# Kernel optimization log

Measured on AMD Instinct MI355X. Metric: run time of the kernel, lower is better.

Reference implementation:

```python
import jax, jax.numpy as jnp
import numpy as np

D_MODEL = 1024
NUM_HEADS = 16
D_K = D_MODEL // NUM_HEADS
B, L = 2, 2048
NEG = -1e9


def setup_inputs() -> dict:
    key = jax.random.key(0)
    ks = jax.random.split(key, 11)
    s = 1.0 / np.sqrt(D_MODEL)
    inp = {
        "Q": jax.random.normal(ks[0], (B, L, D_MODEL), jnp.float32),
        "K": jax.random.normal(ks[1], (B, L, D_MODEL), jnp.float32),
        "V": jax.random.normal(ks[2], (B, L, D_MODEL), jnp.float32),
        # causal mask: True = valid (attend), False = masked
        "mask": jnp.tril(jnp.ones((L, L), bool))[None, None],
        # torch nn.Linear weights stored [out, in]
        "Wq": jax.random.normal(ks[3], (D_MODEL, D_MODEL), jnp.float32) * s,
        "bq": jnp.zeros((D_MODEL,), jnp.float32),
        "Wk": jax.random.normal(ks[4], (D_MODEL, D_MODEL), jnp.float32) * s,
        "bk": jnp.zeros((D_MODEL,), jnp.float32),
        "Wv": jax.random.normal(ks[5], (D_MODEL, D_MODEL), jnp.float32) * s,
        "bv": jnp.zeros((D_MODEL,), jnp.float32),
        "Wo": jax.random.normal(ks[6], (D_MODEL, D_MODEL), jnp.float32) * s,
        "bo": jnp.zeros((D_MODEL,), jnp.float32),
    }
    return inp


def _split_heads(x):  # [B,L,D] -> [B,H,L,d_k]
    b, l, _ = x.shape
    return x.reshape(b, l, NUM_HEADS, D_K).transpose(0, 2, 1, 3)


def reference(Q, K, V, mask, Wq, bq, Wk, bk, Wv, bv, Wo, bo):
    # linear projections (torch Linear: x @ W.T + b)
    q = _split_heads(Q @ Wq.T + bq)
    k = _split_heads(K @ Wk.T + bk)
    v = _split_heads(V @ Wv.T + bv)
    scores = jnp.einsum("bhqd,bhkd->bhqk", q, k) / jnp.sqrt(jnp.float32(D_K))
    scores = jnp.where(mask, scores, NEG)
    probs = jax.nn.softmax(scores, axis=-1)  # dropout inactive at inference
    attn = jnp.einsum("bhqk,bhkd->bhqd", probs, v)
    b, h, l, dk = attn.shape
    o_in = attn.transpose(0, 2, 1, 3).reshape(b, l, D_MODEL)
    return o_in @ Wo.T + bo
```

## Files before the change

kernel.cpp:

```cpp
#include <hip/hip_runtime.h>
#include <stdint.h>

#define D_MODEL 1024
#define NH 16
#define DK 64
#define BBATCH 2
#define LL 2048
#define SCALE_LOG2E 0.1803368801111244f

typedef unsigned short bfu;
typedef __attribute__((ext_vector_type(8))) short bf16x8;
typedef __attribute__((ext_vector_type(4))) float f32x4;

union BF8 { uint32_t w[4]; bf16x8 v; };

__device__ __forceinline__ bfu f2bf(float f) {
    union { float f; uint32_t u; } a; a.f = f;
    uint32_t r = a.u + 0x7FFF + ((a.u >> 16) & 1);
    return (bfu)(r >> 16);
}
__device__ __forceinline__ uint32_t pktrunc(float hi, float lo) {
    return __builtin_amdgcn_perm(__float_as_uint(hi), __float_as_uint(lo), 0x07060302);
}

__device__ __forceinline__ void gload_lds16(const void* g, void* l) {
    __builtin_amdgcn_global_load_lds(
        (const __attribute__((address_space(1))) void*)g,
        (__attribute__((address_space(3))) void*)l, 16, 0, 0);
}

__device__ __forceinline__ int swz(int R, int G) {
    return R * 64 + (((G ^ (R & 7))) << 3);
}

__global__ __launch_bounds__(256) void cvt_all(
    const float4* __restrict__ s0, const float4* __restrict__ s1, const float4* __restrict__ s2,
    const float4* __restrict__ s3, const float4* __restrict__ s4, const float4* __restrict__ s5,
    const float4* __restrict__ s6, ushort4* __restrict__ dst)
{
    int i = blockIdx.x * 256 + threadIdx.x;
    const float4* s; int off;
    float sc = 1.0f;
    if (i < (3 << 20)) {
        int t = i >> 20; s = (t == 0) ? s0 : ((t == 1) ? s1 : s2);
        off = i & ((1 << 20) - 1);
    } else {
        int j = i - (3 << 20);
        int t = j >> 18; s = (t == 0) ? s3 : ((t == 1) ? s4 : ((t == 2) ? s5 : s6));
        if (t == 0) sc = SCALE_LOG2E;
        off = j & ((1 << 18) - 1);
    }
    float4 v = s[off];
    ushort4 o;
    o.x = f2bf(v.x * sc); o.y = f2bf(v.y * sc); o.z = f2bf(v.z * sc); o.w = f2bf(v.w * sc);
    dst[i] = o;
}

#define BM 128
#define BN 128
#define BKK 64

__device__ __forceinline__ int kperm(int k) {
    return (((k >> 4) & 1) << 5) | (((k >> 2) & 3) << 3) | (((k >> 5) & 1) << 2) | (k & 3);
}

__global__ __launch_bounds__(256, 2) void gemm_proj(
    const bfu* __restrict__ Qb, const bfu* __restrict__ Kb, const bfu* __restrict__ Vb,
    const bfu* __restrict__ Wq, const bfu* __restrict__ Wk, const bfu* __restrict__ Wv,
    const float* __restrict__ bq, const float* __restrict__ bk, const float* __restrict__ bv,
    bfu* __restrict__ qp, bfu* __restrict__ kp, bfu* __restrict__ vt)
{
    const int z = blockIdx.z;
    const bfu* A = (z == 0) ? Qb : ((z == 1) ? Kb : Vb);
    const bfu* B = (z == 0) ? Wq : ((z == 1) ? Wk : Wv);
    const float* bias = (z == 0) ? bq : ((z == 1) ? bk : bv);
    const float bsc = (z == 0) ? SCALE_LOG2E : 1.0f;
    bfu* out = (z == 0) ? qp : ((z == 1) ? kp : vt);

    __shared__ __align__(16) bfu As[BM * BKK];
    __shared__ __align__(16) bfu Bs[BN * BKK];

    const int t = threadIdx.x;
    const int lane = t & 63;
    const int wave = t >> 6;
    const int wm = wave & 1, wn = wave >> 1;
    const int tm = blockIdx.y * BM, tn = blockIdx.x * BN;
    const int lr = lane & 15, quad = lane >> 4;

    f32x4 acc[4][4];
    for (int i = 0; i < 4; i++) for (int j = 0; j < 4; j++) acc[i][j] = (f32x4){0.f, 0.f, 0.f, 0.f};

    for (int kt = 0; kt < 1024; kt += BKK) {
        for (int it = 0; it < 4; ++it) {
            int c = t + it * 256;
            int row = c >> 3, gx = (c & 7) ^ (row & 7);
            gload_lds16(&A[(size_t)(tm + row) * 1024 + kt + gx * 8], &As[(size_t)c * 8]);
        }
        for (int it = 0; it < 4; ++it) {
            int c = t + it * 256;
            int row = c >> 3, gx = (c & 7) ^ (row & 7);
            gload_lds16(&B[(size_t)(tn + row) * 1024 + kt + gx * 8], &Bs[(size_t)c * 8]);
        }
        __syncthreads();
        for (int kx = 0; kx < 2; kx++) {
            bf16x8 a[4], b[4];
            for (int i = 0; i < 4; i++)
                a[i] = *(const bf16x8*)&As[swz(wm * 64 + i * 16 + lr, kx * 4 + quad)];
            for (int i = 0; i < 4; i++)
                b[i] = *(const bf16x8*)&Bs[swz(wn * 64 + i * 16 + lr, kx * 4 + quad)];
            for (int mt = 0; mt < 4; mt++)
                for (int nt = 0; nt < 4; nt++)
                    acc[mt][nt] = __builtin_amdgcn_mfma_f32_16x16x32_bf16(a[mt], b[nt], acc[mt][nt], 0, 0, 0);
        }
        __syncthreads();
    }

    for (int mt = 0; mt < 4; mt++)
        for (int nt = 0; nt < 4; nt++)
            for (int r = 0; r < 4; r++) {
                int m = tm + wm * 64 + mt * 16 + quad * 4 + r;
                int n = tn + wn * 64 + nt * 16 + lr;
                float v = acc[mt][nt][r] + bias[n] * bsc;
                int b_ = m >> 11, l = m & 2047;
                int h = n >> 6, d = n & 63;
                if (z < 2)
                    out[((size_t)((b_ * NH + h) * LL + l)) * DK + d] = f2bf(v);
                else {
                    int lp = (l & ~63) | kperm(l & 63);
                    out[((size_t)((b_ * NH + h) * DK + d)) * LL + lp] = f2bf(v);
                }
            }
}

__global__ __launch_bounds__(256, 2) void attn_kernel(
    const bfu* __restrict__ qp, const bfu* __restrict__ kp, const bfu* __restrict__ vtp,
    bfu* __restrict__ attn)
{
    const int id = blockIdx.x;
    const int bh = (id & 7) | (((id >> 3) & 3) << 3);
    const int band = 31 - (id >> 5);
    const int b_ = bh >> 4, h = bh & 15;
    const int t = threadIdx.x;
    const int lane = t & 63, w = t >> 6;
    const int hw = w & 1;
    const int jh = w >> 1;
    const int lr = lane & 15, quad = lane >> 4, q8 = quad << 3;

    __shared__ __align__(16) bfu Ks[2][2][64 * 64];
    __shared__ __align__(16) bfu Vs[2][2][64 * 64];

    const int n  = band + 1;
    const int n0 = (n + 1) >> 1;
    const int nj = (jh == 0) ? n0 : (n - n0);
    const int jb = (jh == 0) ? 0 : n0;

    const int tl = t & 127;
    const int r0 = band * 64 + hw * 32;

    const bfu* kbase = kp + (size_t)bh * LL * DK;
    const bfu* vbase = vtp + (size_t)bh * DK * LL;

    bf16x8 aq[2][2];
    for (int mt = 0; mt < 2; mt++)
        for (int kx = 0; kx < 2; kx++)
            aq[mt][kx] = *(const bf16x8*)&qp[((size_t)bh * LL + r0 + mt * 16 + lr) * DK + kx * 32 + q8];

    f32x4 o[2][4];
    for (int mt = 0; mt < 2; mt++)
        for (int nf = 0; nf < 4; nf++) o[mt][nf] = (f32x4){0.f, 0.f, 0.f, 0.f};
    float lsum[2] = {0.f, 0.f};

    if (nj > 0) {
        for (int it = 0; it < 4; ++it) {
            int c = tl + it * 128;
            int r = c >> 3, gx = (c & 7) ^ (r & 7);
            gload_lds16(&kbase[(size_t)(jb * 64 + r) * DK + gx * 8], &Ks[jh][0][(size_t)c * 8]);
            gload_lds16(&vbase[(size_t)r * LL + jb * 64 + gx * 8], &Vs[jh][0][(size_t)c * 8]);
        }
    }
    __syncthreads();

    for (int i = 0; i < n0; ++i) {
        const int buf = i & 1;
        if (i + 1 < nj) {
            const int nb = buf ^ 1, jn = jb + i + 1;
            for (int it = 0; it < 4; ++it) {
                int c = tl + it * 128;
                int r = c >> 3, gx = (c & 7) ^ (r & 7);
                gload_lds16(&kbase[(size_t)(jn * 64 + r) * DK + gx * 8], &Ks[jh][nb][(size_t)c * 8]);
                gload_lds16(&vbase[(size_t)r * LL + jn * 64 + gx * 8], &Vs[jh][nb][(size_t)c * 8]);
            }
        }
        if (i < nj) {
            const int j = jb + i;
            const bfu* Kt = Ks[jh][buf];
            const bfu* Vt = Vs[jh][buf];
            f32x4 sv[4][2];
            for (int kt = 0; kt < 4; kt++)
                for (int mt = 0; mt < 2; mt++) sv[kt][mt] = (f32x4){0.f, 0.f, 0.f, 0.f};
            for (int kx = 0; kx < 2; kx++)
                for (int kt = 0; kt < 4; kt++) {
                    bf16x8 ak = *(const bf16x8*)&Kt[swz(kt * 16 + lr, kx * 4 + quad)];
                    for (int mt = 0; mt < 2; mt++)
                        sv[kt][mt] = __builtin_amdgcn_mfma_f32_16x16x32_bf16(ak, aq[mt][kx], sv[kt][mt], 0, 0, 0);
                }
            if (j == band) {
                const int mb = r0 & 63;
                for (int kt = 0; kt < 4; kt++)
                    for (int mt = 0; mt < 2; mt++)
                        for (int r = 0; r < 4; r++) {
                            int kl = kt * 16 + quad * 4 + r;
                            int ml = mb + mt * 16 + lr;
                            if (kl > ml) sv[kt][mt][r] = -1e9f;
                        }
            }
            for (int kt = 0; kt < 4; kt++)
                for (int mt = 0; mt < 2; mt++)
                    for (int r = 0; r < 4; r++) {
                        float e = __builtin_amdgcn_exp2f(sv[kt][mt][r]);
                        sv[kt][mt][r] = e;
                        lsum[mt] += e;
                    }
            for (int kx = 0; kx < 2; kx++) {
                BF8 pf[2];
                for (int mt = 0; mt < 2; mt++) {
                    pf[mt].w[0] = pktrunc(sv[kx][mt][1], sv[kx][mt][0]);
                    pf[mt].w[1] = pktrunc(sv[kx][mt][3], sv[kx][mt][2]);
                    pf[mt].w[2] = pktrunc(sv[2 + kx][mt][1], sv[2 + kx][mt][0]);
                    pf[mt].w[3] = pktrunc(sv[2 + kx][mt][3], sv[2 + kx][mt][2]);
                }
                for (int nf = 0; nf < 4; nf++) {
                    bf16x8 av = *(const bf16x8*)&Vt[swz(nf * 16 + lr, kx * 4 + quad)];
                    for (int mt = 0; mt < 2; mt++)
                        o[mt][nf] = __builtin_amdgcn_mfma_f32_16x16x32_bf16(av, pf[mt].v, o[mt][nf], 0, 0, 0);
                }
            }
        }
        __syncthreads();
    }

    float* Of = (float*)&Ks[0][0][0];
    float* Lf = (float*)&Vs[0][0][0];
    const int ci = hw * 64 + lane;
    if (jh == 1) {
        float* dst = Of + ci * 33;
        for (int mt = 0; mt < 2; mt++)
            for (int nf = 0; nf < 4; nf++)
                for (int r = 0; r < 4; r++)
                    dst[mt * 16 + nf * 4 + r] = o[mt][nf][r];
        Lf[ci * 2 + 0] = lsum[0];
        Lf[ci * 2 + 1] = lsum[1];
    }
    __syncthreads();
    if (jh == 0) {
        const float* src = Of + ci * 33;
        for (int mt = 0; mt < 2; mt++)
            for (int nf = 0; nf < 4; nf++)
                for (int r = 0; r < 4; r++)
                    o[mt][nf][r] += src[mt * 16 + nf * 4 + r];
        lsum[0] += Lf[ci * 2 + 0];
        lsum[1] += Lf[ci * 2 + 1];

        for (int mt = 0; mt < 2; mt++) {
            float l = lsum[mt];
            l += __shfl_xor(l, 16);
            l += __shfl_xor(l, 32);
            float rinv = 1.0f / l;
            for (int nf = 0; nf < 4; nf++) {
                uint32_t w0 = ((uint32_t)f2bf(o[mt][nf][1] * rinv) << 16) | f2bf(o[mt][nf][0] * rinv);
                uint32_t w1 = ((uint32_t)f2bf(o[mt][nf][3] * rinv) << 16) | f2bf(o[mt][nf][2] * rinv);
                uint2 pk2 = {w0, w1};
                *(uint2*)&attn[((size_t)(b_ * LL + r0 + mt * 16 + lr)) * D_MODEL + h * DK + nf * 16 + quad * 4] = pk2;
            }
        }
    }
}

#define OBM 128
#define OBN 64

__global__ __launch_bounds__(256) void gemm_out(
    const bfu* __restrict__ A, const bfu* __restrict__ B,
    const float* __restrict__ bias, float* __restrict__ out)
{
    __shared__ __align__(16) bfu As[OBM * 64];
    __shared__ __align__(16) bfu Bs[OBN * 64];

    const int t = threadIdx.x;
    const int lane = t & 63, w = t >> 6;
    const int tm = blockIdx.y * OBM, tn = blockIdx.x * OBN;
    const int lr = lane & 15, quad = lane >> 4;

    f32x4 acc[2][4];
    for (int i = 0; i < 2; i++) for (int j = 0; j < 4; j++) acc[i][j] = (f32x4){0.f, 0.f, 0.f, 0.f};

    for (int kt = 0; kt < 1024; kt += 64) {
        for (int it = 0; it < 4; ++it) {
            int c = t + it * 256;
            int row = c >> 3, gx = (c & 7) ^ (row & 7);
            gload_lds16(&A[(size_t)(tm + row) * 1024 + kt + gx * 8], &As[(size_t)c * 8]);
        }
        for (int it = 0; it < 2; ++it) {
            int c = t + it * 256;
            int row = c >> 3, gx = (c & 7) ^ (row & 7);
            gload_lds16(&B[(size_t)(tn + row) * 1024 + kt + gx * 8], &Bs[(size_t)c * 8]);
        }
        __syncthreads();
        for (int kx = 0; kx < 2; kx++) {
            bf16x8 a[2], b[4];
            for (int mt = 0; mt < 2; mt++)
                a[mt] = *(const bf16x8*)&As[swz(w * 32 + mt * 16 + lr, kx * 4 + quad)];
            for (int nt = 0; nt < 4; nt++)
                b[nt] = *(const bf16x8*)&Bs[swz(nt * 16 + lr, kx * 4 + quad)];
            for (int mt = 0; mt < 2; mt++)
                for (int nt = 0; nt < 4; nt++)
                    acc[mt][nt] = __builtin_amdgcn_mfma_f32_16x16x32_bf16(a[mt], b[nt], acc[mt][nt], 0, 0, 0);
        }
        __syncthreads();
    }

    for (int mt = 0; mt < 2; mt++)
        for (int nt = 0; nt < 4; nt++)
            for (int r = 0; r < 4; r++) {
                int m = tm + w * 32 + mt * 16 + quad * 4 + r;
                int n = tn + nt * 16 + lr;
                out[(size_t)m * D_MODEL + n] = acc[mt][nt][r] + bias[n];
            }
}

extern "C" void kernel_launch(void* const* d_in, const int* in_sizes, int n_in,
                              void* d_out, int out_size, void* d_ws, size_t ws_size,
                              hipStream_t stream) {
    const float* Q  = (const float*)d_in[0];
    const float* K  = (const float*)d_in[1];
    const float* V  = (const float*)d_in[2];
    const float* Wq = (const float*)d_in[4];
    const float* bq = (const float*)d_in[5];
    const float* Wk = (const float*)d_in[6];
    const float* bk = (const float*)d_in[7];
    const float* Wv = (const float*)d_in[8];
    const float* bv = (const float*)d_in[9];
    const float* Wo = (const float*)d_in[10];
    const float* bo = (const float*)d_in[11];
    float* out = (float*)d_out;

    char* ws = (char*)d_ws;
    bfu* Qb  = (bfu*)(ws + ((size_t)0  << 20));
    bfu* Kb  = (bfu*)(ws + ((size_t)8  << 20));
    bfu* Vb  = (bfu*)(ws + ((size_t)16 << 20));
    bfu* Wqb = (bfu*)(ws + ((size_t)24 << 20));
    bfu* Wkb = (bfu*)(ws + ((size_t)26 << 20));
    bfu* Wvb = (bfu*)(ws + ((size_t)28 << 20));
    bfu* Wob = (bfu*)(ws + ((size_t)30 << 20));
    bfu* qp  = (bfu*)(ws + ((size_t)32 << 20));
    bfu* kp  = (bfu*)(ws + ((size_t)40 << 20));
    bfu* vt  = (bfu*)(ws + ((size_t)48 << 20));
    bfu* attn = (bfu*)(ws + ((size_t)56 << 20));

    cvt_all<<<16384, 256, 0, stream>>>(
        (const float4*)Q, (const float4*)K, (const float4*)V,
        (const float4*)Wq, (const float4*)Wk, (const float4*)Wv, (const float4*)Wo,
        (ushort4*)Qb);

    gemm_proj<<<dim3(8, 32, 3), 256, 0, stream>>>(Qb, Kb, Vb, Wqb, Wkb, Wvb,
                                                  bq, bk, bv, qp, kp, vt);

    attn_kernel<<<dim3(1024), 256, 0, stream>>>(qp, kp, vt, attn);

    gemm_out<<<dim3(16, 32), 256, 0, stream>>>(attn, Wob, bo, out);
}
```

Before: 218.9 us.

## Remap GEMM blocks per XCD and single-buffer attention LDS for occupancy

Flattens the projection and output GEMM grids to 1D and remaps block ids so that blocks on the same XCD share rows of A, improving L2 locality. The attention kernel drops K/V double buffering to halve LDS, with launch bounds raised to 4 blocks per CU. Without the overlapped prefetch, each tile load is now exposed, and latency hiding has to come from the extra resident blocks. The higher launch bounds may also force register spills.

Measured after the change: 237.9 us. 8.7% more time.

```diff
diff --git a/kernel.cpp b/kernel.cpp
--- a/kernel.cpp
+++ b/kernel.cpp
@@ -70,7 +70,12 @@
     const float* __restrict__ bq, const float* __restrict__ bk, const float* __restrict__ bv,
     bfu* __restrict__ qp, bfu* __restrict__ kp, bfu* __restrict__ vt)
 {
-    const int z = blockIdx.z;
+    const int id = blockIdx.x;
+    const int xcd = id & 7, q = id >> 3;
+    const int zy = xcd * 12 + (q >> 3);
+    const int x  = q & 7;
+    const int z  = zy >> 5, y = zy & 31;
+
     const bfu* A = (z == 0) ? Qb : ((z == 1) ? Kb : Vb);
     const bfu* B = (z == 0) ? Wq : ((z == 1) ? Wk : Wv);
     const float* bias = (z == 0) ? bq : ((z == 1) ? bk : bv);
@@ -84,7 +89,7 @@
     const int lane = t & 63;
     const int wave = t >> 6;
     const int wm = wave & 1, wn = wave >> 1;
-    const int tm = blockIdx.y * BM, tn = blockIdx.x * BN;
+    const int tm = y * BM, tn = x * BN;
     const int lr = lane & 15, quad = lane >> 4;
 
     f32x4 acc[4][4];
@@ -132,7 +137,7 @@
             }
 }
 
-__global__ __launch_bounds__(256, 2) void attn_kernel(
+__global__ __launch_bounds__(256, 4) void attn_kernel(
     const bfu* __restrict__ qp, const bfu* __restrict__ kp, const bfu* __restrict__ vtp,
     bfu* __restrict__ attn)
 {
@@ -146,8 +151,9 @@
     const int jh = w >> 1;
     const int lr = lane & 15, quad = lane >> 4, q8 = quad << 3;
 
-    __shared__ __align__(16) bfu Ks[2][2][64 * 64];
-    __shared__ __align__(16) bfu Vs[2][2][64 * 64];
+    __shared__ __align__(16) bfu smem[4 * 64 * 64];
+    bfu* Kt = &smem[jh * 4096];
+    bfu* Vt = &smem[(2 + jh) * 4096];
 
     const int n  = band + 1;
     const int n0 = (n + 1) >> 1;
@@ -170,31 +176,20 @@
         for (int nf = 0; nf < 4; nf++) o[mt][nf] = (f32x4){0.f, 0.f, 0.f, 0.f};
     float lsum[2] = {0.f, 0.f};
 
-    if (nj > 0) {
-        for (int it = 0; it < 4; ++it) {
-            int c = tl + it * 128;
-            int r = c >> 3, gx = (c & 7) ^ (r & 7);
-            gload_lds16(&kbase[(size_t)(jb * 64 + r) * DK + gx * 8], &Ks[jh][0][(size_t)c * 8]);
-            gload_lds16(&vbase[(size_t)r * LL + jb * 64 + gx * 8], &Vs[jh][0][(size_t)c * 8]);
-        }
-    }
-    __syncthreads();
-
     for (int i = 0; i < n0; ++i) {
-        const int buf = i & 1;
-        if (i + 1 < nj) {
-            const int nb = buf ^ 1, jn = jb + i + 1;
+        if (i) __syncthreads();
+        if (i < nj) {
+            const int j = jb + i;
             for (int it = 0; it < 4; ++it) {
                 int c = tl + it * 128;
                 int r = c >> 3, gx = (c & 7) ^ (r & 7);
-                gload_lds16(&kbase[(size_t)(jn * 64 + r) * DK + gx * 8], &Ks[jh][nb][(size_t)c * 8]);
-                gload_lds16(&vbase[(size_t)r * LL + jn * 64 + gx * 8], &Vs[jh][nb][(size_t)c * 8]);
-            }
-        }
+                gload_lds16(&kbase[(size_t)(j * 64 + r) * DK + gx * 8], &Kt[(size_t)c * 8]);
+                gload_lds16(&vbase[(size_t)r * LL + j * 64 + gx * 8], &Vt[(size_t)c * 8]);
+            }
+        }
+        __syncthreads();
         if (i < nj) {
             const int j = jb + i;
-            const bfu* Kt = Ks[jh][buf];
-            const bfu* Vt = Vs[jh][buf];
             f32x4 sv[4][2];
             for (int kt = 0; kt < 4; kt++)
                 for (int mt = 0; mt < 2; mt++) sv[kt][mt] = (f32x4){0.f, 0.f, 0.f, 0.f};
@@ -236,11 +231,11 @@
                 }
             }
         }
-        __syncthreads();
-    }
-
-    float* Of = (float*)&Ks[0][0][0];
-    float* Lf = (float*)&Vs[0][0][0];
+    }
+    __syncthreads();
+
+    float* Of = (float*)smem;
+    float* Lf = (float*)smem + 128 * 33;
     const int ci = hw * 64 + lane;
     if (jh == 1) {
         float* dst = Of + ci * 33;
@@ -279,16 +274,21 @@
 #define OBM 128
 #define OBN 64
 
-__global__ __launch_bounds__(256) void gemm_out(
+__global__ __launch_bounds__(256, 4) void gemm_out(
     const bfu* __restrict__ A, const bfu* __restrict__ B,
     const float* __restrict__ bias, float* __restrict__ out)
 {
     __shared__ __align__(16) bfu As[OBM * 64];
     __shared__ __align__(16) bfu Bs[OBN * 64];
 
+    const int id = blockIdx.x;
+    const int xcd = id & 7, q = id >> 3;
+    const int y = xcd * 4 + (q & 3);
+    const int x = q >> 2;
+
     const int t = threadIdx.x;
     const int lane = t & 63, w = t >> 6;
-    const int tm = blockIdx.y * OBM, tn = blockIdx.x * OBN;
+    const int tm = y * OBM, tn = x * OBN;
     const int lr = lane & 15, quad = lane >> 4;
 
     f32x4 acc[2][4];
@@ -362,10 +362,10 @@
         (const float4*)Wq, (const float4*)Wk, (const float4*)Wv, (const float4*)Wo,
         (ushort4*)Qb);
 
-    gemm_proj<<<dim3(8, 32, 3), 256, 0, stream>>>(Qb, Kb, Vb, Wqb, Wkb, Wvb,
-                                                  bq, bk, bv, qp, kp, vt);
+    gemm_proj<<<768, 256, 0, stream>>>(Qb, Kb, Vb, Wqb, Wkb, Wvb,
+                                       bq, bk, bv, qp, kp, vt);
 
     attn_kernel<<<dim3(1024), 256, 0, stream>>>(qp, kp, vt, attn);
 
-    gemm_out<<<dim3(16, 32), 256, 0, stream>>>(attn, Wob, bo, out);
-}
+    gemm_out<<<512, 256, 0, stream>>>(attn, Wob, bo, out);
+}
```

## Fuse fp32-to-bf16 conversion into GEMM tile loads and remap blocks per XCD

Applied to the files above, without the earlier changes.

Removes the separate cvt_all pass by having the projection and output GEMMs read fp32 inputs and weights directly, converting to bf16 in registers before storing to LDS. This drops a full write and re-read of bf16 copies of Q, K, V and the weights, plus one kernel launch. The cost is twice the global bytes per tile load and losing the asynchronous global-to-LDS path, since data now goes through registers. Each weight tile is also re-converted by every block that uses it, and rounding changes from round-to-nearest-even to truncation. The projection grid is flattened to 1D with a mapping that groups each XCD's blocks into contiguous row bands, aiming for better L2 reuse.

Measured after the change: 267.0 us. +22.0%, slower.

```diff
diff --git a/kernel.cpp b/kernel.cpp
--- a/kernel.cpp
+++ b/kernel.cpp
@@ -33,27 +33,15 @@
     return R * 64 + (((G ^ (R & 7))) << 3);
 }
 
-__global__ __launch_bounds__(256) void cvt_all(
-    const float4* __restrict__ s0, const float4* __restrict__ s1, const float4* __restrict__ s2,
-    const float4* __restrict__ s3, const float4* __restrict__ s4, const float4* __restrict__ s5,
-    const float4* __restrict__ s6, ushort4* __restrict__ dst)
-{
-    int i = blockIdx.x * 256 + threadIdx.x;
-    const float4* s; int off;
-    float sc = 1.0f;
-    if (i < (3 << 20)) {
-        int t = i >> 20; s = (t == 0) ? s0 : ((t == 1) ? s1 : s2);
-        off = i & ((1 << 20) - 1);
-    } else {
-        int j = i - (3 << 20);
-        int t = j >> 18; s = (t == 0) ? s3 : ((t == 1) ? s4 : ((t == 2) ? s5 : s6));
-        if (t == 0) sc = SCALE_LOG2E;
-        off = j & ((1 << 18) - 1);
-    }
-    float4 v = s[off];
-    ushort4 o;
-    o.x = f2bf(v.x * sc); o.y = f2bf(v.y * sc); o.z = f2bf(v.z * sc); o.w = f2bf(v.w * sc);
-    dst[i] = o;
+__device__ __forceinline__ uint4 ld8_f32_to_bf16(const float* g, float sc) {
+    const float4* s = (const float4*)g;
+    float4 u = s[0], v = s[1];
+    u.x *= sc; u.y *= sc; u.z *= sc; u.w *= sc;
+    v.x *= sc; v.y *= sc; v.z *= sc; v.w *= sc;
+    uint4 w;
+    w.x = pktrunc(u.y, u.x); w.y = pktrunc(u.w, u.z);
+    w.z = pktrunc(v.y, v.x); w.w = pktrunc(v.w, v.z);
+    return w;
 }
 
 #define BM 128
@@ -65,14 +53,19 @@
 }
 
 __global__ __launch_bounds__(256, 2) void gemm_proj(
-    const bfu* __restrict__ Qb, const bfu* __restrict__ Kb, const bfu* __restrict__ Vb,
-    const bfu* __restrict__ Wq, const bfu* __restrict__ Wk, const bfu* __restrict__ Wv,
+    const float* __restrict__ Qf, const float* __restrict__ Kf, const float* __restrict__ Vf,
+    const float* __restrict__ Wqf, const float* __restrict__ Wkf, const float* __restrict__ Wvf,
     const float* __restrict__ bq, const float* __restrict__ bk, const float* __restrict__ bv,
     bfu* __restrict__ qp, bfu* __restrict__ kp, bfu* __restrict__ vt)
 {
-    const int z = blockIdx.z;
-    const bfu* A = (z == 0) ? Qb : ((z == 1) ? Kb : Vb);
-    const bfu* B = (z == 0) ? Wq : ((z == 1) ? Wk : Wv);
+    const int id = blockIdx.x;
+    const int xcd = id & 7, q = id >> 3;
+    const int zy = xcd * 12 + (q >> 3);
+    const int x  = q & 7;
+    const int z  = zy >> 5, y = zy & 31;
+
+    const float* A = (z == 0) ? Qf : ((z == 1) ? Kf : Vf);
+    const float* B = (z == 0) ? Wqf : ((z == 1) ? Wkf : Wvf);
     const float* bias = (z == 0) ? bq : ((z == 1) ? bk : bv);
     const float bsc = (z == 0) ? SCALE_LOG2E : 1.0f;
     bfu* out = (z == 0) ? qp : ((z == 1) ? kp : vt);
@@ -84,7 +77,7 @@
     const int lane = t & 63;
     const int wave = t >> 6;
     const int wm = wave & 1, wn = wave >> 1;
-    const int tm = blockIdx.y * BM, tn = blockIdx.x * BN;
+    const int tm = y * BM, tn = x * BN;
     const int lr = lane & 15, quad = lane >> 4;
 
     f32x4 acc[4][4];
@@ -94,12 +87,14 @@
         for (int it = 0; it < 4; ++it) {
             int c = t + it * 256;
             int row = c >> 3, gx = (c & 7) ^ (row & 7);
-            gload_lds16(&A[(size_t)(tm + row) * 1024 + kt + gx * 8], &As[(size_t)c * 8]);
+            uint4 w = ld8_f32_to_bf16(&A[(size_t)(tm + row) * 1024 + kt + gx * 8], 1.0f);
+            *(uint4*)&As[(size_t)c * 8] = w;
         }
         for (int it = 0; it < 4; ++it) {
             int c = t + it * 256;
             int row = c >> 3, gx = (c & 7) ^ (row & 7);
-            gload_lds16(&B[(size_t)(tn + row) * 1024 + kt + gx * 8], &Bs[(size_t)c * 8]);
+            uint4 w = ld8_f32_to_bf16(&B[(size_t)(tn + row) * 1024 + kt + gx * 8], bsc);
+            *(uint4*)&Bs[(size_t)c * 8] = w;
         }
         __syncthreads();
         for (int kx = 0; kx < 2; kx++) {
@@ -280,7 +275,7 @@
 #define OBN 64
 
 __global__ __launch_bounds__(256) void gemm_out(
-    const bfu* __restrict__ A, const bfu* __restrict__ B,
+    const bfu* __restrict__ A, const float* __restrict__ B,
     const float* __restrict__ bias, float* __restrict__ out)
 {
     __shared__ __align__(16) bfu As[OBM * 64];
@@ -303,7 +298,8 @@
         for (int it = 0; it < 2; ++it) {
             int c = t + it * 256;
             int row = c >> 3, gx = (c & 7) ^ (row & 7);
-            gload_lds16(&B[(size_t)(tn + row) * 1024 + kt + gx * 8], &Bs[(size_t)c * 8]);
+            uint4 wv = ld8_f32_to_bf16(&B[(size_t)(tn + row) * 1024 + kt + gx * 8], 1.0f);
+            *(uint4*)&Bs[(size_t)c * 8] = wv;
         }
         __syncthreads();
         for (int kx = 0; kx < 2; kx++) {
@@ -345,27 +341,15 @@
     float* out = (float*)d_out;
 
     char* ws = (char*)d_ws;
-    bfu* Qb  = (bfu*)(ws + ((size_t)0  << 20));
-    bfu* Kb  = (bfu*)(ws + ((size_t)8  << 20));
-    bfu* Vb  = (bfu*)(ws + ((size_t)16 << 20));
-    bfu* Wqb = (bfu*)(ws + ((size_t)24 << 20));
-    bfu* Wkb = (bfu*)(ws + ((size_t)26 << 20));
-    bfu* Wvb = (bfu*)(ws + ((size_t)28 << 20));
-    bfu* Wob = (bfu*)(ws + ((size_t)30 << 20));
-    bfu* qp  = (bfu*)(ws + ((size_t)32 << 20));
-    bfu* kp  = (bfu*)(ws + ((size_t)40 << 20));
-    bfu* vt  = (bfu*)(ws + ((size_t)48 << 20));
-    bfu* attn = (bfu*)(ws + ((size_t)56 << 20));
-
-    cvt_all<<<16384, 256, 0, stream>>>(
-        (const float4*)Q, (const float4*)K, (const float4*)V,
-        (const float4*)Wq, (const float4*)Wk, (const float4*)Wv, (const float4*)Wo,
-        (ushort4*)Qb);
-
-    gemm_proj<<<dim3(8, 32, 3), 256, 0, stream>>>(Qb, Kb, Vb, Wqb, Wkb, Wvb,
-                                                  bq, bk, bv, qp, kp, vt);
+    bfu* qp  = (bfu*)(ws + ((size_t)0  << 20));
+    bfu* kp  = (bfu*)(ws + ((size_t)8  << 20));
+    bfu* vt  = (bfu*)(ws + ((size_t)16 << 20));
+    bfu* attn = (bfu*)(ws + ((size_t)24 << 20));
+
+    gemm_proj<<<768, 256, 0, stream>>>(Q, K, V, Wq, Wk, Wv,
+                                       bq, bk, bv, qp, kp, vt);
 
     attn_kernel<<<dim3(1024), 256, 0, stream>>>(qp, kp, vt, attn);
 
-    gemm_out<<<dim3(16, 32), 256, 0, stream>>>(attn, Wob, bo, out);
-}
+    gemm_out<<<dim3(16, 32), 256, 0, stream>>>(attn, Wo, bo, out);
+}
```
